# Kernel optimization log

Measured on AMD Instinct MI355X. Metric: run time of the kernel, lower is better.

## Reference

```python
import jax, jax.numpy as jnp
import numpy as np

TEMPERATURE = 8.0  # sqrt(d_head=64)
NEG_INF = -1e15


def setup_inputs() -> dict:
    key = jax.random.key(0)
    k1, k2_, k3, k4, k5, k6 = jax.random.split(key, 6)
    BH, N, D = 16, 2048, 64
    B = 2  # edge batch; BH // B == 8 heads
    return {
        "q": jax.random.normal(k1, (BH, N, D), dtype=jnp.float32),
        "k": jax.random.normal(k2_, (BH, N, D), dtype=jnp.float32),
        "v": jax.random.normal(k3, (BH, N, D), dtype=jnp.float32),
        "k2": jax.random.normal(k4, (BH, N, D), dtype=jnp.float32),
        "mask": jax.random.randint(k5, (BH, 1, N), 0, 2) > 0,
        "edge": jax.random.randint(k6, (B, N, N), 0, 2).astype(jnp.int32),
    }


def reference(q, k, v, k2, mask, edge):
    # attn scores: [bh, n, m]
    attn = jnp.einsum("bnd,bmd->bnm", q, k) / TEMPERATURE
    # torch .repeat along dim0 == tile
    reps = attn.shape[0] // edge.shape[0]
    edge_t = jnp.tile(edge, (reps, 1, 1))
    attn = jnp.where(edge_t == 0, NEG_INF, attn)
    attn = jnp.where(mask, NEG_INF, attn)
    attn = jax.nn.softmax(attn, axis=2)  # dropout p=0 (eval)
    output = jnp.einsum("bnm,bmd->bnd", attn, v)
    # non_linear=False, so no sigmoid
    return (output, attn)
```

## Files before the change

### kernel.cpp

```cpp
#include <hip/hip_runtime.h>
#include <stdint.h>
#include <math.h>

#define BH_ 16
#define N_  2048
#define D_  64
#define NEGV (-1e15f)

typedef __attribute__((ext_vector_type(8))) short bf16x8;
typedef __attribute__((ext_vector_type(8))) unsigned short us8;
typedef __attribute__((ext_vector_type(4))) float f32x4;

#define OFF_MASKU8 0u
#define OFF_MBITS  32768u
#define OFF_EBITS  65536u
#define OFF_QBF    1114112u
#define OFF_KBF    5308416u
#define OFF_VT     9502720u
#define WS_V6      13697024u

#define BARRIER_LGKM() do {                                   \
    asm volatile("s_waitcnt lgkmcnt(0)" ::: "memory");        \
    __builtin_amdgcn_sched_barrier(0);                        \
    __builtin_amdgcn_s_barrier();                             \
    __builtin_amdgcn_sched_barrier(0);                        \
} while (0)

__device__ __forceinline__ unsigned short f2bf(float f) {
    unsigned u = __float_as_uint(f);
    return (unsigned short)((u + 0x7FFFu + ((u >> 16) & 1u)) >> 16);
}

__global__ __launch_bounds__(256)
void prep_all(const float* __restrict__ q, const float* __restrict__ k,
              const float* __restrict__ v, const void* __restrict__ mraw,
              const int* __restrict__ edge,
              unsigned short* __restrict__ qbf, unsigned short* __restrict__ kbf,
              unsigned short* __restrict__ vT,
              unsigned short* __restrict__ e16, unsigned long long* __restrict__ mbits)
{
    __shared__ unsigned short shbuf[64][72];
    __shared__ int flag;
    const int bid = blockIdx.x;
    const int t   = threadIdx.x;

    if (bid < 2048) {
        const int idx = bid * 256 + t;
        const int4* p = (const int4*)(edge + (size_t)idx * 16);
        unsigned m = 0;
        #pragma unroll
        for (int i = 0; i < 4; ++i) {
            const int4 vv = p[i];
            m |= (vv.x != 0 ? 1u : 0u) << (i * 4 + 0);
            m |= (vv.y != 0 ? 1u : 0u) << (i * 4 + 1);
            m |= (vv.z != 0 ? 1u : 0u) << (i * 4 + 2);
            m |= (vv.w != 0 ? 1u : 0u) << (i * 4 + 3);
        }
        e16[idx] = (unsigned short)m;
    } else if (bid < 2560) {
        const int b2 = bid - 2048;
        const int rt = b2 & 31, bh = b2 >> 5;
        const size_t base = ((size_t)bh * N_ + (size_t)rt * 64) * D_;
        #pragma unroll
        for (int i = 0; i < 4; ++i) {
            const int idx = t + i * 256;
            float4 f = *(const float4*)(q + base + (size_t)idx * 4);
            ushort4 s; s.x = f2bf(f.x); s.y = f2bf(f.y); s.z = f2bf(f.z); s.w = f2bf(f.w);
            *(ushort4*)(qbf + base + (size_t)idx * 4) = s;
            f = *(const float4*)(k + base + (size_t)idx * 4);
            s.x = f2bf(f.x); s.y = f2bf(f.y); s.z = f2bf(f.z); s.w = f2bf(f.w);
            *(ushort4*)(kbf + base + (size_t)idx * 4) = s;
            f = *(const float4*)(v + base + (size_t)idx * 4);
            const int row = idx >> 4;
            const int d0  = (idx & 15) * 4;
            shbuf[d0 + 0][row] = f2bf(f.x);
            shbuf[d0 + 1][row] = f2bf(f.y);
            shbuf[d0 + 2][row] = f2bf(f.z);
            shbuf[d0 + 3][row] = f2bf(f.w);
        }
        __syncthreads();
        const int d  = t >> 2;
        const int c4 = (t & 3) * 16;
        const size_t ob = ((size_t)bh * D_ + d) * N_ + (size_t)rt * 64 + c4;
        *(us8*)(vT + ob)     = *(us8*)&shbuf[d][c4];
        *(us8*)(vT + ob + 8) = *(us8*)&shbuf[d][c4 + 8];
    } else {
        const int bh = bid - 2560;
        if (t == 0) flag = 0;
        __syncthreads();
        const int* mi = (const int*)mraw;
        int bad = 0;
        for (int i = t; i < 8192; i += 256)
            if ((unsigned)mi[i] > 1u) bad = 1;
        if (bad) atomicOr(&flag, 1);
        __syncthreads();
        const int is_u8 = flag;
        const uint8_t* m8 = (const uint8_t*)mraw;
        const int w4 = t >> 6, l = t & 63;
        for (int it = 0; it < 8; ++it) {
            const int pos = bh * 2048 + it * 256 + w4 * 64 + l;
            const bool on = is_u8 ? (m8[pos] != 0) : (mi[pos] != 0);
            unsigned long long bal = __ballot(on);
            if (l == 0) mbits[bh * 32 + it * 4 + w4] = bal;
        }
    }
}

__global__ __launch_bounds__(256)
void attn_v8(const unsigned short* __restrict__ qbf,
             const unsigned short* __restrict__ kbf,
             const unsigned short* __restrict__ vT,
             const unsigned long long* __restrict__ ebits,
             const unsigned long long* __restrict__ mbits,
             float* __restrict__ out, float* __restrict__ attn)
{
    __shared__ unsigned short sK[2][4096];
    __shared__ unsigned short sV[2][4096];
    __shared__ char pbuf[4][2048];

    const int bh   = blockIdx.x;
    const int tile = blockIdx.y;
    const int t    = threadIdx.x;
    const int w    = t >> 6;
    const int lane = t & 63;
    const int l15  = lane & 15;
    const int lg   = lane >> 4;
    const int rbase = tile * 64;
    const int myrow = rbase + w * 16 + l15;

    const unsigned short* qb = qbf + (size_t)bh * N_ * D_;
    const unsigned short* kb = kbf + (size_t)bh * N_ * D_;
    const unsigned short* vb = vT  + (size_t)bh * D_ * N_;
    const unsigned long long* ebrow =
        ebits + ((size_t)(bh & 1) * N_ + (size_t)myrow) * 32;
    const unsigned long long* mb = mbits + bh * 32;
    float* outb = out + (size_t)bh * N_ * D_;
    float* arow = attn + (size_t)bh * N_ * N_ + (size_t)myrow * N_ + lg * 4;

    const bf16x8 aq0 = *(const bf16x8*)(qb + (size_t)myrow * D_ + lg * 8);
    const bf16x8 aq1 = *(const bf16x8*)(qb + (size_t)myrow * D_ + lg * 8 + 32);

    const int s0row = t >> 3;
    const int s1row = s0row + 32;
    const int t8    = t & 7;
    const int ds0 = s0row * 64 + ((t8 ^ (s0row & 7)) * 8);
    const int ds1 = s1row * 64 + ((t8 ^ (s1row & 7)) * 8);

    {
        const us8 a0 = *(const us8*)(kb + (size_t)t * 8);
        const us8 a1 = *(const us8*)(kb + (size_t)(t + 256) * 8);
        *(us8*)(sK[0] + ds0) = a0;
        *(us8*)(sK[0] + ds1) = a1;
        BARRIER_LGKM();
    }
    float lacc = 0.f;
    #pragma unroll 1
    for (int kc = 0; kc < 32; ++kc) {
        const int cur = kc & 1;
        us8 nk0, nk1;
        if (kc < 31) {
            const unsigned short* s = kb + (size_t)(kc + 1) * 4096;
            nk0 = *(const us8*)(s + (size_t)t * 8);
            nk1 = *(const us8*)(s + (size_t)(t + 256) * 8);
        }
        const unsigned long long wbits = ebrow[kc] & ~mb[kc];
        const unsigned short* kcur = sK[cur];
        #pragma unroll
        for (int nt = 0; nt < 4; ++nt) {
            const int row = nt * 16 + l15, sw = row & 7;
            const bf16x8 k0 = *(const bf16x8*)(kcur + row * 64 + ((lg ^ sw) * 8));
            const bf16x8 k1 = *(const bf16x8*)(kcur + row * 64 + (((lg + 4) ^ sw) * 8));
            f32x4 c = (f32x4){0.f, 0.f, 0.f, 0.f};
            c = __builtin_amdgcn_mfma_f32_16x16x32_bf16(k0, aq0, c, 0, 0, 0);
            c = __builtin_amdgcn_mfma_f32_16x16x32_bf16(k1, aq1, c, 0, 0, 0);
            const unsigned bits = (unsigned)(wbits >> (nt * 16 + lg * 4)) & 0xFu;
            #pragma unroll
            for (int r = 0; r < 4; ++r)
                lacc += ((bits >> r) & 1u) ? __expf(c[r] * 0.125f) : 0.f;
        }
        if (kc < 31) {
            *(us8*)(sK[cur ^ 1] + ds0) = nk0;
            *(us8*)(sK[cur ^ 1] + ds1) = nk1;
        }
        BARRIER_LGKM();
    }
    lacc += __shfl_xor(lacc, 16);
    lacc += __shfl_xor(lacc, 32);
    const float inv = 1.0f / lacc;

    {
        const us8 a0 = *(const us8*)(kb + (size_t)t * 8);
        const us8 a1 = *(const us8*)(kb + (size_t)(t + 256) * 8);
        const us8 b0 = *(const us8*)(vb + (size_t)s0row * 2048 + t8 * 8);
        const us8 b1 = *(const us8*)(vb + (size_t)s1row * 2048 + t8 * 8);
        *(us8*)(sK[0] + ds0) = a0;
        *(us8*)(sK[0] + ds1) = a1;
        *(us8*)(sV[0] + ds0) = b0;
        *(us8*)(sV[0] + ds1) = b1;
        BARRIER_LGKM();
    }

    f32x4 o[4];
    #pragma unroll
    for (int nt = 0; nt < 4; ++nt) o[nt] = (f32x4){0.f, 0.f, 0.f, 0.f};

    char* pbw = pbuf[w];
    const int swzP = (l15 & 7) << 4;
    const int ab0 = (l15 * 128 + lg * 16)      ^ swzP;
    const int ab1 = (l15 * 128 + lg * 16 + 64) ^ swzP;

    #pragma unroll 1
    for (int kc = 0; kc < 32; ++kc) {
        const int cur = kc & 1;
        us8 nk0, nk1, nv0, nv1;
        if (kc < 31) {
            const unsigned short* srck = kb + (size_t)(kc + 1) * 4096;
            const unsigned short* srcv = vb + (size_t)(kc + 1) * 64;
            nk0 = *(const us8*)(srck + (size_t)t * 8);
            nk1 = *(const us8*)(srck + (size_t)(t + 256) * 8);
            nv0 = *(const us8*)(srcv + (size_t)s0row * 2048 + t8 * 8);
            nv1 = *(const us8*)(srcv + (size_t)s1row * 2048 + t8 * 8);
        }
        const unsigned long long wbits = ebrow[kc] & ~mb[kc];
        const unsigned short* kcur = sK[cur];
        float4 ev[4];
        #pragma unroll
        for (int nt = 0; nt < 4; ++nt) {
            const int row = nt * 16 + l15, sw = row & 7;
            const bf16x8 k0 = *(const bf16x8*)(kcur + row * 64 + ((lg ^ sw) * 8));
            const bf16x8 k1 = *(const bf16x8*)(kcur + row * 64 + (((lg + 4) ^ sw) * 8));
            f32x4 c = (f32x4){0.f, 0.f, 0.f, 0.f};
            c = __builtin_amdgcn_mfma_f32_16x16x32_bf16(k0, aq0, c, 0, 0, 0);
            c = __builtin_amdgcn_mfma_f32_16x16x32_bf16(k1, aq1, c, 0, 0, 0);
            const unsigned bits = (unsigned)(wbits >> (nt * 16 + lg * 4)) & 0xFu;
            float4 e;
            e.x = (bits & 1u) ? __expf(c[0] * 0.125f) * inv : 0.f;
            e.y = (bits & 2u) ? __expf(c[1] * 0.125f) * inv : 0.f;
            e.z = (bits & 4u) ? __expf(c[2] * 0.125f) * inv : 0.f;
            e.w = (bits & 8u) ? __expf(c[3] * 0.125f) * inv : 0.f;
            ev[nt] = e;
            ushort4 pe;
            pe.x = f2bf(e.x); pe.y = f2bf(e.y); pe.z = f2bf(e.z); pe.w = f2bf(e.w);
            const int wbyte = (l15 * 128 + nt * 32 + lg * 8) ^ swzP;
            *(ushort4*)(pbw + wbyte) = pe;
        }
        const bf16x8 ap0 = *(const bf16x8*)(pbw + ab0);
        const bf16x8 ap1 = *(const bf16x8*)(pbw + ab1);
        const unsigned short* vcur = sV[cur];
        #pragma unroll
        for (int nt = 0; nt < 4; ++nt) {
            const int row = nt * 16 + l15, sw = row & 7;
            const bf16x8 bv0 = *(const bf16x8*)(vcur + row * 64 + ((lg ^ sw) * 8));
            const bf16x8 bv1 = *(const bf16x8*)(vcur + row * 64 + (((lg + 4) ^ sw) * 8));
            o[nt] = __builtin_amdgcn_mfma_f32_16x16x32_bf16(ap0, bv0, o[nt], 0, 0, 0);
            o[nt] = __builtin_amdgcn_mfma_f32_16x16x32_bf16(ap1, bv1, o[nt], 0, 0, 0);
        }
        {
            float* astore = arow + kc * 64;
            #pragma unroll
            for (int nt = 0; nt < 4; ++nt)
                *(float4*)(astore + nt * 16) = ev[nt];
        }
        if (kc < 31) {
            *(us8*)(sK[cur ^ 1] + ds0) = nk0;
            *(us8*)(sK[cur ^ 1] + ds1) = nk1;
            *(us8*)(sV[cur ^ 1] + ds0) = nv0;
            *(us8*)(sV[cur ^ 1] + ds1) = nv1;
        }
        BARRIER_LGKM();
    }

    #pragma unroll
    for (int nt = 0; nt < 4; ++nt)
        #pragma unroll
        for (int r = 0; r < 4; ++r)
            outb[(size_t)(rbase + w * 16 + lg * 4 + r) * D_ + nt * 16 + l15] = o[nt][r];
}

__global__ __launch_bounds__(256)
void normalize_mask(const void* __restrict__ mask_raw, uint8_t* __restrict__ mask_out)
{
    __shared__ int is_u8;
    const int t = threadIdx.x;
    if (t == 0) is_u8 = 0;
    __syncthreads();
    const int* mi = (const int*)mask_raw;
    int bad = 0;
    for (int i = t; i < 8192; i += 256)
        if ((unsigned)mi[i] > 1u) bad = 1;
    if (bad) atomicOr(&is_u8, 1);
    __syncthreads();
    const int total = BH_ * N_;
    if (is_u8) {
        const uint8_t* m8 = (const uint8_t*)mask_raw;
        for (int i = t; i < total; i += 256) mask_out[i] = m8[i] ? 1 : 0;
    } else {
        for (int i = t; i < total; i += 256) mask_out[i] = (uint8_t)mi[i];
    }
}

__global__ __launch_bounds__(256)
void attn_fused(const float* __restrict__ q, const float* __restrict__ k,
                const float* __restrict__ v, const uint8_t* __restrict__ mask,
                const int* __restrict__ edge, float* __restrict__ out,
                float* __restrict__ attn)
{
    __shared__ float qsT[D_][64 + 4];
    __shared__ float kt [D_][64 + 4];
    __shared__ float vs [64][D_ + 4];
    const int tile = blockIdx.x, bh = blockIdx.y, t = threadIdx.x;
    const int rg = t >> 4, cg = t & 15, r0 = rg * 4, c0 = cg * 4;
    const int row_base = tile * 64;
    const float* qb = q + (size_t)bh * N_ * D_;
    const float* kb = k + (size_t)bh * N_ * D_;
    const float* vb = v + (size_t)bh * N_ * D_;
    const uint8_t* mbp = mask + (size_t)bh * N_;
    const int* ebp = edge + (size_t)(bh & 1) * N_ * N_;
    float* outb = out + (size_t)bh * N_ * D_;
    float* attnb = attn + (size_t)bh * N_ * N_;
    {
        const int rr = t >> 2, dblk = (t & 3) * 16;
        const float* src = qb + (size_t)(row_base + rr) * D_ + dblk;
        #pragma unroll
        for (int qq = 0; qq < 4; ++qq) {
            float4 val = *(const float4*)(src + qq * 4);
            qsT[dblk + qq*4 + 0][rr] = val.x; qsT[dblk + qq*4 + 1][rr] = val.y;
            qsT[dblk + qq*4 + 2][rr] = val.z; qsT[dblk + qq*4 + 3][rr] = val.w;
        }
    }
    float m_i[4], l_i[4];
    #pragma unroll
    for (int i = 0; i < 4; ++i) { m_i[i] = -INFINITY; l_i[i] = 0.f; }
    for (int kc = 0; kc < 32; ++kc) {
        __syncthreads();
        {
            const int ccr = t >> 2, dblk = (t & 3) * 16;
            const float* src = kb + (size_t)(kc * 64 + ccr) * D_ + dblk;
            #pragma unroll
            for (int qq = 0; qq < 4; ++qq) {
                float4 val = *(const float4*)(src + qq * 4);
                kt[dblk + qq*4 + 0][ccr] = val.x; kt[dblk + qq*4 + 1][ccr] = val.y;
                kt[dblk + qq*4 + 2][ccr] = val.z; kt[dblk + qq*4 + 3][ccr] = val.w;
            }
        }
        __syncthreads();
        float sc[4][4];
        #pragma unroll
        for (int i = 0; i < 4; ++i) { sc[i][0]=sc[i][1]=sc[i][2]=sc[i][3]=0.f; }
        for (int d = 0; d < D_; ++d) {
            const float4 qv = *(const float4*)&qsT[d][r0];
            const float4 kv = *(const float4*)&kt[d][c0];
            #pragma unroll
            for (int i = 0; i < 4; ++i) {
                const float qi = (i==0)?qv.x:(i==1)?qv.y:(i==2)?qv.z:qv.w;
                sc[i][0] = fmaf(qi, kv.x, sc[i][0]); sc[i][1] = fmaf(qi, kv.y, sc[i][1]);
                sc[i][2] = fmaf(qi, kv.z, sc[i][2]); sc[i][3] = fmaf(qi, kv.w, sc[i][3]);
            }
        }
        const int cbase = kc * 64 + c0;
        const uint8_t m0 = mbp[cbase], m1 = mbp[cbase+1], m2 = mbp[cbase+2], m3 = mbp[cbase+3];
        #pragma unroll
        for (int i = 0; i < 4; ++i) {
            const int rglob = row_base + r0 + i;
            const int4 e4 = *(const int4*)(ebp + (size_t)rglob * N_ + cbase);
            float s0 = sc[i][0]*0.125f, s1 = sc[i][1]*0.125f, s2 = sc[i][2]*0.125f, s3 = sc[i][3]*0.125f;
            if (e4.x == 0 || m0) s0 = NEGV; if (e4.y == 0 || m1) s1 = NEGV;
            if (e4.z == 0 || m2) s2 = NEGV; if (e4.w == 0 || m3) s3 = NEGV;
            float cmax = fmaxf(fmaxf(s0,s1), fmaxf(s2,s3));
            cmax = fmaxf(cmax, __shfl_xor(cmax,1)); cmax = fmaxf(cmax, __shfl_xor(cmax,2));
            cmax = fmaxf(cmax, __shfl_xor(cmax,4)); cmax = fmaxf(cmax, __shfl_xor(cmax,8));
            const float nm = fmaxf(m_i[i], cmax);
            float ss = __expf(s0-nm)+__expf(s1-nm)+__expf(s2-nm)+__expf(s3-nm);
            ss += __shfl_xor(ss,1); ss += __shfl_xor(ss,2); ss += __shfl_xor(ss,4); ss += __shfl_xor(ss,8);
            l_i[i] = l_i[i]*__expf(m_i[i]-nm) + ss; m_i[i] = nm;
        }
    }
    float inv_l[4];
    #pragma unroll
    for (int i = 0; i < 4; ++i) inv_l[i] = 1.0f / l_i[i];
    float oacc[4][4];
    #pragma unroll
    for (int i = 0; i < 4; ++i) { oacc[i][0]=oacc[i][1]=oacc[i][2]=oacc[i][3]=0.f; }
    for (int kc = 0; kc < 32; ++kc) {
        __syncthreads();
        {
            const int ccr = t >> 2, dblk = (t & 3) * 16;
            const float* src = kb + (size_t)(kc * 64 + ccr) * D_ + dblk;
            #pragma unroll
            for (int qq = 0; qq < 4; ++qq) {
                float4 val = *(const float4*)(src + qq * 4);
                kt[dblk + qq*4 + 0][ccr] = val.x; kt[dblk + qq*4 + 1][ccr] = val.y;
                kt[dblk + qq*4 + 2][ccr] = val.z; kt[dblk + qq*4 + 3][ccr] = val.w;
            }
            const float* srcv = vb + (size_t)(kc * 64 + ccr) * D_ + dblk;
            #pragma unroll
            for (int qq = 0; qq < 4; ++qq)
                *(float4*)&vs[ccr][dblk + qq * 4] = *(const float4*)(srcv + qq * 4);
        }
        __syncthreads();
        float sc[4][4];
        #pragma unroll
        for (int i = 0; i < 4; ++i) { sc[i][0]=sc[i][1]=sc[i][2]=sc[i][3]=0.f; }
        for (int d = 0; d < D_; ++d) {
            const float4 qv = *(const float4*)&qsT[d][r0];
            const float4 kv = *(const float4*)&kt[d][c0];
            #pragma unroll
            for (int i = 0; i < 4; ++i) {
                const float qi = (i==0)?qv.x:(i==1)?qv.y:(i==2)?qv.z:qv.w;
                sc[i][0] = fmaf(qi, kv.x, sc[i][0]); sc[i][1] = fmaf(qi, kv.y, sc[i][1]);
                sc[i][2] = fmaf(qi, kv.z, sc[i][2]); sc[i][3] = fmaf(qi, kv.w, sc[i][3]);
            }
        }
        const int cbase = kc * 64 + c0;
        const uint8_t m0 = mbp[cbase], m1 = mbp[cbase+1], m2 = mbp[cbase+2], m3 = mbp[cbase+3];
        float p[4][4];
        #pragma unroll
        for (int i = 0; i < 4; ++i) {
            const int rglob = row_base + r0 + i;
            const int4 e4 = *(const int4*)(ebp + (size_t)rglob * N_ + cbase);
            float s0 = sc[i][0]*0.125f, s1 = sc[i][1]*0.125f, s2 = sc[i][2]*0.125f, s3 = sc[i][3]*0.125f;
            if (e4.x == 0 || m0) s0 = NEGV; if (e4.y == 0 || m1) s1 = NEGV;
            if (e4.z == 0 || m2) s2 = NEGV; if (e4.w == 0 || m3) s3 = NEGV;
            p[i][0] = __expf(s0-m_i[i])*inv_l[i]; p[i][1] = __expf(s1-m_i[i])*inv_l[i];
            p[i][2] = __expf(s2-m_i[i])*inv_l[i]; p[i][3] = __expf(s3-m_i[i])*inv_l[i];
            *(float4*)&attnb[(size_t)rglob * N_ + cbase] = make_float4(p[i][0],p[i][1],p[i][2],p[i][3]);
        }
        __syncthreads();
        #pragma unroll
        for (int i = 0; i < 4; ++i)
            *(float4*)&kt[r0 + i][c0] = make_float4(p[i][0],p[i][1],p[i][2],p[i][3]);
        __syncthreads();
        for (int c4 = 0; c4 < 64; c4 += 4) {
            float prr[4][4];
            #pragma unroll
            for (int i = 0; i < 4; ++i) {
                const float4 tmp = *(const float4*)&kt[r0 + i][c4];
                prr[i][0]=tmp.x; prr[i][1]=tmp.y; prr[i][2]=tmp.z; prr[i][3]=tmp.w;
            }
            #pragma unroll
            for (int cc = 0; cc < 4; ++cc) {
                const float4 vv = *(const float4*)&vs[c4 + cc][c0];
                #pragma unroll
                for (int i = 0; i < 4; ++i) {
                    oacc[i][0] = fmaf(prr[i][cc], vv.x, oacc[i][0]);
                    oacc[i][1] = fmaf(prr[i][cc], vv.y, oacc[i][1]);
                    oacc[i][2] = fmaf(prr[i][cc], vv.z, oacc[i][2]);
                    oacc[i][3] = fmaf(prr[i][cc], vv.w, oacc[i][3]);
                }
            }
        }
    }
    #pragma unroll
    for (int i = 0; i < 4; ++i)
        *(float4*)&outb[(size_t)(row_base + r0 + i) * D_ + c0] =
            make_float4(oacc[i][0], oacc[i][1], oacc[i][2], oacc[i][3]);
}

extern "C" void kernel_launch(void* const* d_in, const int* in_sizes, int n_in,
                              void* d_out, int out_size, void* d_ws, size_t ws_size,
                              hipStream_t stream) {
    const float* q    = (const float*)d_in[0];
    const float* k    = (const float*)d_in[1];
    const float* v    = (const float*)d_in[2];
    const void*  mraw = d_in[4];
    const int*   edge = (const int*)d_in[5];

    float* out  = (float*)d_out;
    float* attn = (float*)d_out + (size_t)BH_ * N_ * D_;

    char* ws = (char*)d_ws;

    if (ws_size < (size_t)WS_V6) {
        uint8_t* mask_u8 = (uint8_t*)(ws + OFF_MASKU8);
        normalize_mask<<<1, 256, 0, stream>>>(mraw, mask_u8);
        attn_fused<<<dim3(32, 16), 256, 0, stream>>>(q, k, v, mask_u8, edge, out, attn);
        return;
    }

    unsigned long long* mbits = (unsigned long long*)(ws + OFF_MBITS);
    unsigned short*     e16   = (unsigned short*)(ws + OFF_EBITS);
    unsigned short*     qbf   = (unsigned short*)(ws + OFF_QBF);
    unsigned short*     kbf   = (unsigned short*)(ws + OFF_KBF);
    unsigned short*     vT    = (unsigned short*)(ws + OFF_VT);

    prep_all<<<dim3(2576), 256, 0, stream>>>(q, k, v, mraw, edge,
                                             qbf, kbf, vT, e16, mbits);
    attn_v8<<<dim3(BH_, N_ / 64), 256, 0, stream>>>(
        qbf, kbf, vT, (const unsigned long long*)e16, mbits, out, attn);
}
```

Before: 121.1 us.

## Stash unnormalized bf16 probabilities in workspace to skip QK recompute in PV pass

Adds a new attention kernel whose first pass computes masked exp scores and writes them as bf16 to a large workspace buffer, along with the row sums. The second pass reads those stored values back instead of recomputing QK^T, writes the normalized fp32 attention matrix, and feeds the bf16 values directly into the PV MFMA, scaling the output by the inverse sum at the end. This removes the second QK matmul and its K tile staging, but adds about 128MB of extra global writes and reads. It only runs when the provided workspace is large enough; otherwise the old kernel is used.

```diff
diff --git a/kernel.cpp b/kernel.cpp
--- a/kernel.cpp
+++ b/kernel.cpp
@@ -18,6 +18,8 @@
 #define OFF_KBF    5308416u
 #define OFF_VT     9502720u
 #define WS_V6      13697024u
+#define OFF_PU     13697024u
+#define WS_V10     147914752u
 
 #define BARRIER_LGKM() do {                                   \
     asm volatile("s_waitcnt lgkmcnt(0)" ::: "memory");        \
@@ -29,6 +31,9 @@
 __device__ __forceinline__ unsigned short f2bf(float f) {
     unsigned u = __float_as_uint(f);
     return (unsigned short)((u + 0x7FFFu + ((u >> 16) & 1u)) >> 16);
+}
+__device__ __forceinline__ float bf2f(short s) {
+    return __uint_as_float(((unsigned)(unsigned short)s) << 16);
 }
 
 __global__ __launch_bounds__(256)
@@ -107,6 +112,162 @@
 }
 
 __global__ __launch_bounds__(256)
+void attn_v10(const unsigned short* __restrict__ qbf,
+              const unsigned short* __restrict__ kbf,
+              const unsigned short* __restrict__ vT,
+              const unsigned long long* __restrict__ ebits,
+              const unsigned long long* __restrict__ mbits,
+              unsigned short* __restrict__ pu,
+              float* __restrict__ out, float* __restrict__ attn)
+{
+    __shared__ unsigned short sKV[2][4096];
+    __shared__ float invA[4][16];
+
+    const int bh   = blockIdx.x;
+    const int tile = blockIdx.y;
+    const int t    = threadIdx.x;
+    const int w    = t >> 6;
+    const int lane = t & 63;
+    const int l15  = lane & 15;
+    const int lg   = lane >> 4;
+    const int rbase = tile * 64;
+    const int myrow = rbase + w * 16 + l15;
+
+    const unsigned short* qb = qbf + (size_t)bh * N_ * D_;
+    const unsigned short* kb = kbf + (size_t)bh * N_ * D_;
+    const unsigned short* vb = vT  + (size_t)bh * D_ * N_;
+    const unsigned long long* ebrow =
+        ebits + ((size_t)(bh & 1) * N_ + (size_t)myrow) * 32;
+    const unsigned long long* mb = mbits + bh * 32;
+    float* outb = out + (size_t)bh * N_ * D_;
+    float* arow = attn + ((size_t)bh * N_ + myrow) * N_;
+    unsigned short* purow = pu + ((size_t)bh * N_ + myrow) * N_;
+
+    const bf16x8 aq0 = *(const bf16x8*)(qb + (size_t)myrow * D_ + lg * 8);
+    const bf16x8 aq1 = *(const bf16x8*)(qb + (size_t)myrow * D_ + lg * 8 + 32);
+
+    const int s0row = t >> 3;
+    const int s1row = s0row + 32;
+    const int t8    = t & 7;
+    const int ds0 = s0row * 64 + ((t8 ^ (s0row & 7)) * 8);
+    const int ds1 = s1row * 64 + ((t8 ^ (s1row & 7)) * 8);
+
+    {
+        *(us8*)(sKV[0] + ds0) = *(const us8*)(kb + (size_t)t * 8);
+        *(us8*)(sKV[0] + ds1) = *(const us8*)(kb + (size_t)(t + 256) * 8);
+        BARRIER_LGKM();
+    }
+    float lacc = 0.f;
+    #pragma unroll 1
+    for (int kc = 0; kc < 32; ++kc) {
+        const int cur = kc & 1;
+        us8 nk0, nk1;
+        if (kc < 31) {
+            const unsigned short* s = kb + (size_t)(kc + 1) * 4096;
+            nk0 = *(const us8*)(s + (size_t)t * 8);
+            nk1 = *(const us8*)(s + (size_t)(t + 256) * 8);
+        }
+        const unsigned long long wbits = ebrow[kc] & ~mb[kc];
+        const unsigned short* kcur = sKV[cur];
+        #pragma unroll
+        for (int nt = 0; nt < 4; ++nt) {
+            const int row = nt * 16 + l15, sw = row & 7;
+            const bf16x8 k0 = *(const bf16x8*)(kcur + row * 64 + ((lg ^ sw) * 8));
+            const bf16x8 k1 = *(const bf16x8*)(kcur + row * 64 + (((lg + 4) ^ sw) * 8));
+            f32x4 c = (f32x4){0.f, 0.f, 0.f, 0.f};
+            c = __builtin_amdgcn_mfma_f32_16x16x32_bf16(k0, aq0, c, 0, 0, 0);
+            c = __builtin_amdgcn_mfma_f32_16x16x32_bf16(k1, aq1, c, 0, 0, 0);
+            const unsigned bits = (unsigned)(wbits >> (nt * 16 + lg * 4)) & 0xFu;
+            const float e0 = (bits & 1u) ? __expf(c[0] * 0.125f) : 0.f;
+            const float e1 = (bits & 2u) ? __expf(c[1] * 0.125f) : 0.f;
+            const float e2 = (bits & 4u) ? __expf(c[2] * 0.125f) : 0.f;
+            const float e3 = (bits & 8u) ? __expf(c[3] * 0.125f) : 0.f;
+            lacc += (e0 + e1) + (e2 + e3);
+            ushort4 pe;
+            pe.x = f2bf(e0); pe.y = f2bf(e1); pe.z = f2bf(e2); pe.w = f2bf(e3);
+            *(ushort4*)(purow + kc * 64 + nt * 16 + lg * 4) = pe;
+        }
+        if (kc < 31) {
+            *(us8*)(sKV[cur ^ 1] + ds0) = nk0;
+            *(us8*)(sKV[cur ^ 1] + ds1) = nk1;
+        }
+        BARRIER_LGKM();
+    }
+    lacc += __shfl_xor(lacc, 16);
+    lacc += __shfl_xor(lacc, 32);
+    const float inv = 1.0f / lacc;
+    if (lg == 0) invA[w][l15] = inv;
+
+    asm volatile("s_waitcnt vmcnt(0)" ::: "memory");
+    __builtin_amdgcn_sched_barrier(0);
+
+    {
+        *(us8*)(sKV[0] + ds0) = *(const us8*)(vb + (size_t)s0row * 2048 + t8 * 8);
+        *(us8*)(sKV[0] + ds1) = *(const us8*)(vb + (size_t)s1row * 2048 + t8 * 8);
+        BARRIER_LGKM();
+    }
+
+    f32x4 o[4];
+    #pragma unroll
+    for (int nt = 0; nt < 4; ++nt) o[nt] = (f32x4){0.f, 0.f, 0.f, 0.f};
+
+    #pragma unroll 1
+    for (int kc = 0; kc < 32; ++kc) {
+        const int cur = kc & 1;
+        us8 nv0, nv1;
+        if (kc < 31) {
+            const unsigned short* srcv = vb + (size_t)(kc + 1) * 64;
+            nv0 = *(const us8*)(srcv + (size_t)s0row * 2048 + t8 * 8);
+            nv1 = *(const us8*)(srcv + (size_t)s1row * 2048 + t8 * 8);
+        }
+        const bf16x8 ap0 = *(const bf16x8*)(purow + kc * 64 + lg * 8);
+        const bf16x8 ap1 = *(const bf16x8*)(purow + kc * 64 + lg * 8 + 32);
+        {
+            float4 f0, f1, f2, f3;
+            f0.x = bf2f(ap0[0]) * inv; f0.y = bf2f(ap0[1]) * inv;
+            f0.z = bf2f(ap0[2]) * inv; f0.w = bf2f(ap0[3]) * inv;
+            f1.x = bf2f(ap0[4]) * inv; f1.y = bf2f(ap0[5]) * inv;
+            f1.z = bf2f(ap0[6]) * inv; f1.w = bf2f(ap0[7]) * inv;
+            f2.x = bf2f(ap1[0]) * inv; f2.y = bf2f(ap1[1]) * inv;
+            f2.z = bf2f(ap1[2]) * inv; f2.w = bf2f(ap1[3]) * inv;
+            f3.x = bf2f(ap1[4]) * inv; f3.y = bf2f(ap1[5]) * inv;
+            f3.z = bf2f(ap1[6]) * inv; f3.w = bf2f(ap1[7]) * inv;
+            float* astore = arow + kc * 64 + lg * 8;
+            *(float4*)(astore)      = f0;
+            *(float4*)(astore + 4)  = f1;
+            *(float4*)(astore + 32) = f2;
+            *(float4*)(astore + 36) = f3;
+        }
+        const unsigned short* vcur = sKV[cur];
+        #pragma unroll
+        for (int nt = 0; nt < 4; ++nt) {
+            const int row = nt * 16 + l15, sw = row & 7;
+            const bf16x8 bv0 = *(const bf16x8*)(vcur + row * 64 + ((lg ^ sw) * 8));
+            const bf16x8 bv1 = *(const bf16x8*)(vcur + row * 64 + (((lg + 4) ^ sw) * 8));
+            o[nt] = __builtin_amdgcn_mfma_f32_16x16x32_bf16(ap0, bv0, o[nt], 0, 0, 0);
+            o[nt] = __builtin_amdgcn_mfma_f32_16x16x32_bf16(ap1, bv1, o[nt], 0, 0, 0);
+        }
+        if (kc < 31) {
+            *(us8*)(sKV[cur ^ 1] + ds0) = nv0;
+            *(us8*)(sKV[cur ^ 1] + ds1) = nv1;
+        }
+        BARRIER_LGKM();
+    }
+
+    const float i0 = invA[w][lg * 4 + 0];
+    const float i1 = invA[w][lg * 4 + 1];
+    const float i2 = invA[w][lg * 4 + 2];
+    const float i3 = invA[w][lg * 4 + 3];
+    #pragma unroll
+    for (int nt = 0; nt < 4; ++nt) {
+        outb[(size_t)(rbase + w * 16 + lg * 4 + 0) * D_ + nt * 16 + l15] = o[nt][0] * i0;
+        outb[(size_t)(rbase + w * 16 + lg * 4 + 1) * D_ + nt * 16 + l15] = o[nt][1] * i1;
+        outb[(size_t)(rbase + w * 16 + lg * 4 + 2) * D_ + nt * 16 + l15] = o[nt][2] * i2;
+        outb[(size_t)(rbase + w * 16 + lg * 4 + 3) * D_ + nt * 16 + l15] = o[nt][3] * i3;
+    }
+}
+
+__global__ __launch_bounds__(256)
 void attn_v8(const unsigned short* __restrict__ qbf,
              const unsigned short* __restrict__ kbf,
              const unsigned short* __restrict__ vT,
@@ -147,10 +308,8 @@
     const int ds1 = s1row * 64 + ((t8 ^ (s1row & 7)) * 8);
 
     {
-        const us8 a0 = *(const us8*)(kb + (size_t)t * 8);
-        const us8 a1 = *(const us8*)(kb + (size_t)(t + 256) * 8);
-        *(us8*)(sK[0] + ds0) = a0;
-        *(us8*)(sK[0] + ds1) = a1;
+        *(us8*)(sK[0] + ds0) = *(const us8*)(kb + (size_t)t * 8);
+        *(us8*)(sK[0] + ds1) = *(const us8*)(kb + (size_t)(t + 256) * 8);
         BARRIER_LGKM();
     }
     float lacc = 0.f;
@@ -189,14 +348,10 @@
     const float inv = 1.0f / lacc;
 
     {
-        const us8 a0 = *(const us8*)(kb + (size_t)t * 8);
-        const us8 a1 = *(const us8*)(kb + (size_t)(t + 256) * 8);
-        const us8 b0 = *(const us8*)(vb + (size_t)s0row * 2048 + t8 * 8);
-        const us8 b1 = *(const us8*)(vb + (size_t)s1row * 2048 + t8 * 8);
-        *(us8*)(sK[0] + ds0) = a0;
-        *(us8*)(sK[0] + ds1) = a1;
-        *(us8*)(sV[0] + ds0) = b0;
-        *(us8*)(sV[0] + ds1) = b1;
+        *(us8*)(sK[0] + ds0) = *(const us8*)(kb + (size_t)t * 8);
+        *(us8*)(sK[0] + ds1) = *(const us8*)(kb + (size_t)(t + 256) * 8);
+        *(us8*)(sV[0] + ds0) = *(const us8*)(vb + (size_t)s0row * 2048 + t8 * 8);
+        *(us8*)(sV[0] + ds1) = *(const us8*)(vb + (size_t)s1row * 2048 + t8 * 8);
         BARRIER_LGKM();
     }
 
@@ -485,6 +640,13 @@
 
     prep_all<<<dim3(2576), 256, 0, stream>>>(q, k, v, mraw, edge,
                                              qbf, kbf, vT, e16, mbits);
-    attn_v8<<<dim3(BH_, N_ / 64), 256, 0, stream>>>(
-        qbf, kbf, vT, (const unsigned long long*)e16, mbits, out, attn);
-}
+
+    if (ws_size >= (size_t)WS_V10) {
+        unsigned short* pu = (unsigned short*)(ws + OFF_PU);
+        attn_v10<<<dim3(BH_, N_ / 64), 256, 0, stream>>>(
+            qbf, kbf, vT, (const unsigned long long*)e16, mbits, pu, out, attn);
+    } else {
+        attn_v8<<<dim3(BH_, N_ / 64), 256, 0, stream>>>(
+            qbf, kbf, vT, (const unsigned long long*)e16, mbits, out, attn);
+    }
+}
```

After: 176.6 us. +45.8%, slower.
